# Performance work log

Hardware: AMD Instinct MI355X
Metric: run time of the kernel (lower is better)

Reference implementation:

```python
import jax, jax.numpy as jnp
import numpy as np

GN_EPS = 1e-5
G = 8          # SKA groups
SKS3 = 27      # sks**3


def _aff(x, s, b):
    # folded BatchNorm (eval): per-channel scale + shift on NCDHW tensor
    return x * s[None, :, None, None, None] + b[None, :, None, None, None]


def _c1(x, w):
    # 1x1x1 conv as channel GEMM; w: [O, I]
    return jnp.einsum('bcdhw,oc->bodhw', x, w)


def _dw5(x, w):
    # depthwise 5x5x5 conv, pad=2; w: [C, 1, 5, 5, 5]
    return jax.lax.conv_general_dilated(
        x, w, window_strides=(1, 1, 1), padding=[(2, 2)] * 3,
        dimension_numbers=('NCDHW', 'OIDHW', 'NCDHW'),
        feature_group_count=x.shape[1])


def setup_inputs() -> dict:
    key = jax.random.key(0)
    ks = jax.random.split(key, 24)
    B, C, D, H, W = 2, 64, 32, 32, 32

    def n(k, shape, scale=1.0):
        return jax.random.normal(k, shape, jnp.float32) * scale

    def u(k, shape):
        return jax.random.uniform(k, shape, jnp.float32, 0.5, 1.5)

    return {
        'x': n(ks[0], (B, C, D, H, W)),
        'w1': n(ks[1], (32, 64), 64 ** -0.5),
        's1': u(ks[2], (32,)), 'b1': n(ks[3], (32,), 0.1),
        'w2': n(ks[4], (32, 1, 5, 5, 5), 125 ** -0.5),
        's2': u(ks[5], (32,)), 'b2': n(ks[6], (32,), 0.1),
        'w3': n(ks[7], (32, 32), 32 ** -0.5),
        's3': u(ks[8], (32,)), 'b3': n(ks[9], (32,), 0.1),
        'w4': n(ks[10], (216, 32), 32 ** -0.5), 'b4': n(ks[11], (216,), 0.1),
        'gn_g': u(ks[12], (216,)), 'gn_b': n(ks[13], (216,), 0.1),
        'bn_s': u(ks[14], (64,)), 'bn_b': n(ks[15], (64,), 0.1),
        'pw1_w': n(ks[16], (128, 64), 64 ** -0.5),
        'pw1_s': u(ks[17], (128,)), 'pw1_b': n(ks[18], (128,), 0.1),
        'pw2_w': n(ks[19], (64, 128), 128 ** -0.5),
        'pw2_s': u(ks[20], (64,)), 'pw2_b': n(ks[21], (64,), 0.1),
    }


def reference(x, w1, s1, b1, w2, s2, b2, w3, s3, b3, w4, b4,
              gn_g, gn_b, bn_s, bn_b,
              pw1_w, pw1_s, pw1_b, pw2_w, pw2_s, pw2_b):
    B, C, D, H, W = x.shape

    # ---- LKP3D: dynamic kernel generation ----
    a = jax.nn.relu(_aff(_c1(x, w1), s1, b1))          # cv1 + BN + ReLU
    a = _aff(_dw5(a, w2), s2, b2)                      # cv2 (5^3 dw) + BN
    a = jax.nn.relu(_aff(_c1(a, w3), s3, b3))          # cv3 + BN + ReLU
    wk = _c1(a, w4) + b4[None, :, None, None, None]    # cv4: [B,216,D,H,W]
    # GroupNorm: num_groups = dim//groups = 8, channels = 216
    g = wk.reshape(B, G, SKS3, D, H, W)
    mu = g.mean(axis=(2, 3, 4, 5), keepdims=True)
    var = g.var(axis=(2, 3, 4, 5), keepdims=True)
    g = (g - mu) * jax.lax.rsqrt(var + GN_EPS)
    wk = g.reshape(B, G * SKS3, D, H, W) * gn_g[None, :, None, None, None] \
         + gn_b[None, :, None, None, None]
    wk = wk.reshape(B, G, SKS3, D, H, W)               # [B, G, 27, D, H, W]

    # ---- SKA3D: apply dynamic kernels (27 shifted copies, grouped) ----
    offs = [(di, hi, wi) for di in (-1, 0, 1) for hi in (-1, 0, 1) for wi in (-1, 0, 1)]
    patches = jnp.stack(
        [jnp.roll(x, (-di, -hi, -wi), axis=(2, 3, 4)) for di, hi, wi in offs],
        axis=2)                                        # [B, C, 27, D, H, W]
    p = patches.reshape(B, G, C // G, SKS3, D, H, W)
    sk = jnp.einsum('bgckdhw,bgkdhw->bgcdhw', p, wk).reshape(B, C, D, H, W)

    y = _aff(sk, bn_s, bn_b) + x                       # LSConv BN + residual

    # ---- FFN (residual): pw1 + BN + ReLU + pw2 + BN ----
    f = jax.nn.relu(_aff(_c1(y, pw1_w), pw1_s, pw1_b))
    f = _aff(_c1(f, pw2_w), pw2_s, pw2_b)
    return y + f
```

## Files before the change

kernel.cpp:

```cpp
#include <hip/hip_runtime.h>

#define SPAT 32768
#define BATCH 2
#define GN_EPS 1e-5f

__device__ __forceinline__ void fma4(float4& a, const float4& v, float w) {
    a.x = fmaf(v.x, w, a.x); a.y = fmaf(v.y, w, a.y);
    a.z = fmaf(v.z, w, a.z); a.w = fmaf(v.w, w, a.w);
}

template <int CIN, int NO, bool RELU, bool AFF>
__global__ __launch_bounds__(256) void k_c1(
    const float* __restrict__ in, const float* __restrict__ w,
    const float* __restrict__ sc, const float* __restrict__ bi,
    float* __restrict__ out, int Cout)
{
    int q = blockIdx.x * 256 + threadIdx.x;
    int s = q * 4;
    int o0 = blockIdx.y * NO, b = blockIdx.z;
    const float* ip = in + (size_t)b * CIN * SPAT + s;
    float4 acc[NO];
#pragma unroll
    for (int i = 0; i < NO; ++i) acc[i] = {0.f, 0.f, 0.f, 0.f};
#pragma unroll 4
    for (int c = 0; c < CIN; ++c) {
        float4 v = *(const float4*)(ip + (size_t)c * SPAT);
#pragma unroll
        for (int i = 0; i < NO; ++i)
            fma4(acc[i], v, w[(o0 + i) * CIN + c]);
    }
#pragma unroll
    for (int i = 0; i < NO; ++i) {
        int o = o0 + i;
        float scale = AFF ? sc[o] : 1.f;
        float shift = bi[o];
        float4 r = acc[i];
        r.x = r.x * scale + shift; r.y = r.y * scale + shift;
        r.z = r.z * scale + shift; r.w = r.w * scale + shift;
        if (RELU) {
            r.x = fmaxf(r.x, 0.f); r.y = fmaxf(r.y, 0.f);
            r.z = fmaxf(r.z, 0.f); r.w = fmaxf(r.w, 0.f);
        }
        *(float4*)(out + ((size_t)b * Cout + o) * SPAT + s) = r;
    }
}

__global__ __launch_bounds__(256) void k_gram(
    const float* __restrict__ a, float* __restrict__ partial)
{
    __shared__ float lds[32 * 257];
    int blk = blockIdx.x, b = blockIdx.z;
    const float* ap = a + (size_t)b * 32 * SPAT + blk * 256;
    for (int i = threadIdx.x; i < 32 * 64; i += 256) {
        int m = i >> 6, p4 = (i & 63) * 4;
        float4 v = *(const float4*)(ap + (size_t)m * SPAT + p4);
        lds[m * 257 + p4 + 0] = v.x; lds[m * 257 + p4 + 1] = v.y;
        lds[m * 257 + p4 + 2] = v.z; lds[m * 257 + p4 + 3] = v.w;
    }
    __syncthreads();
    float* outp = partial + (size_t)(b * 128 + blk) * 1056;
#pragma unroll
    for (int it = 0; it < 4; ++it) {
        int pid = threadIdx.x + it * 256;
        const float* pa = &lds[(pid >> 5) * 257];
        const float* pb = &lds[(pid & 31) * 257];
        float acc = 0.f;
#pragma unroll 8
        for (int p = 0; p < 256; ++p) acc = fmaf(pa[p], pb[p], acc);
        outp[pid] = acc;
    }
    if (threadIdx.x < 32) {
        const float* pa = &lds[threadIdx.x * 257];
        float scc = 0.f;
#pragma unroll 8
        for (int p = 0; p < 256; ++p) scc += pa[p];
        outp[1024 + threadIdx.x] = scc;
    }
}

__global__ __launch_bounds__(512) void k_stats(
    const float* __restrict__ partial, const float* __restrict__ w4,
    const float* __restrict__ b4, float* __restrict__ stats)
{
    __shared__ float G[2 * 1056];
    __shared__ float sred[432], ssred[432];
    for (int e = threadIdx.x; e < 2 * 1056; e += 512) {
        int b = e / 1056, pid = e % 1056;
        float acc = 0.f;
#pragma unroll 8
        for (int blk = 0; blk < 128; ++blk)
            acc += partial[(size_t)(b * 128 + blk) * 1056 + pid];
        G[e] = acc;
    }
    __syncthreads();
    if (threadIdx.x < 432) {
        int t = threadIdx.x;
        int b = t / 216, r = t % 216, g = r / 27, k = r % 27;
        const float* wk = w4 + (g * 27 + k) * 32;
        float wreg[32];
#pragma unroll
        for (int m = 0; m < 32; ++m) wreg[m] = wk[m];
        const float* Gb = &G[b * 1056];
        const float* Sb = &G[b * 1056 + 1024];
        float sk = 0.f, ssk = 0.f;
#pragma unroll
        for (int m = 0; m < 32; ++m) {
            sk = fmaf(wreg[m], Sb[m], sk);
            float dot = 0.f;
#pragma unroll
            for (int mm = 0; mm < 32; ++mm)
                dot = fmaf(wreg[mm], Gb[m * 32 + mm], dot);
            ssk = fmaf(wreg[m], dot, ssk);
        }
        float bb = b4[g * 27 + k];
        float NN = (float)SPAT;
        ssk += 2.f * bb * sk + NN * bb * bb;
        sk  += NN * bb;
        sred[t] = sk; ssred[t] = ssk;
    }
    __syncthreads();
    if (threadIdx.x < 16) {
        int bg = threadIdx.x;
        float s = 0.f, ss = 0.f;
        for (int k = 0; k < 27; ++k) { s += sred[bg * 27 + k]; ss += ssred[bg * 27 + k]; }
        float N27 = 27.f * (float)SPAT;
        float mu = s / N27;
        float var = ss / N27 - mu * mu;
        stats[bg * 2 + 0] = mu;
        stats[bg * 2 + 1] = rsqrtf(var + GN_EPS);
    }
}

__global__ __launch_bounds__(256) void k_ska(
    const float* __restrict__ x, const float* __restrict__ wk,
    const float* __restrict__ stats,
    const float* __restrict__ gn_g, const float* __restrict__ gn_b,
    const float* __restrict__ bn_s, const float* __restrict__ bn_b,
    float* __restrict__ y)
{
    int q = blockIdx.x * 256 + threadIdx.x;
    int s = q * 4;
    int g = blockIdx.y, b = blockIdx.z;
    int bg = b * 8 + g;
    float mu  = stats[bg * 2 + 0];
    float inv = stats[bg * 2 + 1];
    int d = s >> 10, h = (s >> 5) & 31, w0 = s & 31;
    int lane = threadIdx.x & 63;
    int xl_src = (lane & 56) | ((lane + 7) & 7);
    int xr_src = (lane & 56) | ((lane + 1) & 7);
    const float* xg = x + ((size_t)(b * 64 + g * 8)) * SPAT;
    const float* wp = wk + ((size_t)(b * 216 + g * 27)) * SPAT + s;

    float4 acc[8];
    float4 xc[8];
#pragma unroll
    for (int c = 0; c < 8; ++c) acc[c] = {0.f, 0.f, 0.f, 0.f};

#pragma unroll
    for (int kd = 0; kd < 3; ++kd) {
        int zd = (d + kd + 31) & 31;
#pragma unroll
        for (int kh = 0; kh < 3; ++kh) {
            int zh = (h + kh + 31) & 31;
            int kbase = (kd * 3 + kh) * 3;
            float wn[3][4];
#pragma unroll
            for (int kw = 0; kw < 3; ++kw) {
                int kk = kbase + kw;
                float4 wq = *(const float4*)(wp + (size_t)kk * SPAT);
                float A = gn_g[g * 27 + kk] * inv;
                float B = gn_b[g * 27 + kk] - mu * A;
                wn[kw][0] = wq.x * A + B;
                wn[kw][1] = wq.y * A + B;
                wn[kw][2] = wq.z * A + B;
                wn[kw][3] = wq.w * A + B;
            }
            int rowoff = zd * 1024 + zh * 32;
            bool center = (kd == 1) && (kh == 1);
#pragma unroll
            for (int c = 0; c < 8; ++c) {
                float4 m = *(const float4*)(xg + (size_t)c * SPAT + rowoff + w0);
                if (center) xc[c] = m;
                float xl = __shfl(m.w, xl_src, 64);
                float xr = __shfl(m.x, xr_src, 64);
                float win[6] = {xl, m.x, m.y, m.z, m.w, xr};
#pragma unroll
                for (int kw = 0; kw < 3; ++kw) {
                    acc[c].x = fmaf(win[0 + kw], wn[kw][0], acc[c].x);
                    acc[c].y = fmaf(win[1 + kw], wn[kw][1], acc[c].y);
                    acc[c].z = fmaf(win[2 + kw], wn[kw][2], acc[c].z);
                    acc[c].w = fmaf(win[3 + kw], wn[kw][3], acc[c].w);
                }
            }
        }
    }
#pragma unroll
    for (int c = 0; c < 8; ++c) {
        int ch = g * 8 + c;
        float bs = bn_s[ch], bb = bn_b[ch];
        float4 r;
        r.x = acc[c].x * bs + bb + xc[c].x;
        r.y = acc[c].y * bs + bb + xc[c].y;
        r.z = acc[c].z * bs + bb + xc[c].z;
        r.w = acc[c].w * bs + bb + xc[c].w;
        *(float4*)(y + ((size_t)(b * 64 + ch)) * SPAT + s) = r;
    }
}

__global__ __launch_bounds__(256) void k_dw5(
    const float* __restrict__ in, const float* __restrict__ w2,
    const float* __restrict__ s2, const float* __restrict__ b2,
    float* __restrict__ out)
{
    __shared__ float lds[8 * 36 * 40];
    int tid = threadIdx.x;
    int d0 = blockIdx.x * 4;
    int c = blockIdx.y, b = blockIdx.z;
    const float* ip = in + ((size_t)(b * 32 + c)) * SPAT;

    float4 z = {0.f, 0.f, 0.f, 0.f};
    for (int i = tid; i < 8 * 36 * 40 / 4; i += 256)
        ((float4*)lds)[i] = z;
    __syncthreads();
    for (int i = tid; i < 8 * 256; i += 256) {
        int p = i >> 8, rem = i & 255;
        int r = rem >> 3, c4 = (rem & 7) * 4;
        int d = d0 - 2 + p;
        if (d >= 0 && d < 32) {
            float4 v = *(const float4*)(ip + d * 1024 + r * 32 + c4);
            *(float4*)&lds[p * 1440 + (r + 2) * 40 + (c4 + 4)] = v;
        }
    }
    __syncthreads();

    float scl = s2[c], shf = b2[c];
    const float* wt = w2 + c * 125;
#pragma unroll
    for (int k = 0; k < 4; ++k) {
        int j = tid + k * 256;
        int pd = j >> 8, rem = j & 255;
        int hr = rem >> 3, w4i = (rem & 7) * 4;
        float4 acc = {0.f, 0.f, 0.f, 0.f};
#pragma unroll
        for (int kd = 0; kd < 5; ++kd) {
            const float* pl = &lds[(pd + kd) * 1440];
#pragma unroll
            for (int kh = 0; kh < 5; ++kh) {
                const float* row = pl + (hr + kh) * 40 + w4i;
                float4 r0 = *(const float4*)(row);
                float4 r1 = *(const float4*)(row + 4);
                float4 r2 = *(const float4*)(row + 8);
                float win[12] = {r0.x, r0.y, r0.z, r0.w,
                                 r1.x, r1.y, r1.z, r1.w,
                                 r2.x, r2.y, r2.z, r2.w};
#pragma unroll
                for (int kw = 0; kw < 5; ++kw) {
                    float wv = wt[kd * 25 + kh * 5 + kw];
                    acc.x = fmaf(wv, win[2 + 0 + kw], acc.x);
                    acc.y = fmaf(wv, win[2 + 1 + kw], acc.y);
                    acc.z = fmaf(wv, win[2 + 2 + kw], acc.z);
                    acc.w = fmaf(wv, win[2 + 3 + kw], acc.w);
                }
            }
        }
        acc.x = acc.x * scl + shf; acc.y = acc.y * scl + shf;
        acc.z = acc.z * scl + shf; acc.w = acc.w * scl + shf;
        *(float4*)(out + ((size_t)(b * 32 + c)) * SPAT
                   + (d0 + pd) * 1024 + hr * 32 + w4i) = acc;
    }
}

template <int NO>
__global__ __launch_bounds__(256) void k_pw2_out(
    const float* __restrict__ f1, const float* __restrict__ w,
    const float* __restrict__ sc, const float* __restrict__ bi,
    const float* __restrict__ yres, float* __restrict__ out)
{
    int q = blockIdx.x * 256 + threadIdx.x;
    int s = q * 4;
    int o0 = blockIdx.y * NO, b = blockIdx.z;
    const float* ip = f1 + (size_t)b * 128 * SPAT + s;
    float4 acc[NO];
#pragma unroll
    for (int i = 0; i < NO; ++i) acc[i] = {0.f, 0.f, 0.f, 0.f};
#pragma unroll 4
    for (int c = 0; c < 128; ++c) {
        float4 v = *(const float4*)(ip + (size_t)c * SPAT);
#pragma unroll
        for (int i = 0; i < NO; ++i)
            fma4(acc[i], v, w[(o0 + i) * 128 + c]);
    }
#pragma unroll
    for (int i = 0; i < NO; ++i) {
        int o = o0 + i;
        float scale = sc[o], shift = bi[o];
        float4 yv = *(const float4*)(yres + ((size_t)(b * 64 + o)) * SPAT + s);
        float4 r = acc[i];
        r.x = r.x * scale + shift + yv.x;
        r.y = r.y * scale + shift + yv.y;
        r.z = r.z * scale + shift + yv.z;
        r.w = r.w * scale + shift + yv.w;
        *(float4*)(out + ((size_t)(b * 64 + o)) * SPAT + s) = r;
    }
}

extern "C" void kernel_launch(void* const* d_in, const int* in_sizes, int n_in,
                              void* d_out, int out_size, void* d_ws, size_t ws_size,
                              hipStream_t stream)
{
    const float* x     = (const float*)d_in[0];
    const float* w1    = (const float*)d_in[1];
    const float* s1    = (const float*)d_in[2];
    const float* b1    = (const float*)d_in[3];
    const float* w2    = (const float*)d_in[4];
    const float* s2    = (const float*)d_in[5];
    const float* b2    = (const float*)d_in[6];
    const float* w3    = (const float*)d_in[7];
    const float* s3    = (const float*)d_in[8];
    const float* b3    = (const float*)d_in[9];
    const float* w4    = (const float*)d_in[10];
    const float* b4    = (const float*)d_in[11];
    const float* gn_g  = (const float*)d_in[12];
    const float* gn_b  = (const float*)d_in[13];
    const float* bn_s  = (const float*)d_in[14];
    const float* bn_b  = (const float*)d_in[15];
    const float* pw1_w = (const float*)d_in[16];
    const float* pw1_s = (const float*)d_in[17];
    const float* pw1_b = (const float*)d_in[18];
    const float* pw2_w = (const float*)d_in[19];
    const float* pw2_s = (const float*)d_in[20];
    const float* pw2_b = (const float*)d_in[21];

    float* ws    = (float*)d_ws;
    float* a1    = ws;
    float* a2    = a1 + (size_t)BATCH * 32 * SPAT;
    float* yb    = ws;
    float* wkb   = ws + (size_t)BATCH * 64 * SPAT;
    float* f1    = wkb;
    float* part  = wkb + (size_t)BATCH * 216 * SPAT;
    float* stats = part + (size_t)256 * 1056;

    dim3 blk(256);
    k_c1<64, 4, true, true><<<dim3(SPAT / 1024, 8, BATCH), blk, 0, stream>>>(
        x, w1, s1, b1, a1, 32);
    k_dw5<<<dim3(8, 32, BATCH), blk, 0, stream>>>(a1, w2, s2, b2, a2);
    k_c1<32, 4, true, true><<<dim3(SPAT / 1024, 8, BATCH), blk, 0, stream>>>(
        a2, w3, s3, b3, a1, 32);
    k_gram<<<dim3(128, 1, BATCH), blk, 0, stream>>>(a1, part);
    k_stats<<<dim3(1), dim3(512), 0, stream>>>(part, w4, b4, stats);
    k_c1<32, 8, false, false><<<dim3(SPAT / 1024, 27, BATCH), blk, 0, stream>>>(
        a1, w4, nullptr, b4, wkb, 216);
    k_ska<<<dim3(SPAT / 1024, 8, BATCH), blk, 0, stream>>>(
        x, wkb, stats, gn_g, gn_b, bn_s, bn_b, yb);
    k_c1<64, 8, true, true><<<dim3(SPAT / 1024, 16, BATCH), blk, 0, stream>>>(
        yb, pw1_w, pw1_s, pw1_b, f1, 128);
    k_pw2_out<8><<<dim3(SPAT / 1024, 8, BATCH), blk, 0, stream>>>(
        f1, pw2_w, pw2_s, pw2_b, yb, (float*)d_out);
}
```

Baseline: 270.2 us.

## Fuse cv4 dynamic-kernel generation into SKA kernel via shared memory

The cv4 1x1 conv that produced the 216-channel dynamic kernel tensor is now computed inside the SKA kernel. Each block computes its group's 27 normalized weights for 512 voxels into LDS, then applies them. This removes writing and re-reading the large wk buffer from global memory. It costs an extra kernel-weight GEMM per block, about 55KB of LDS per block (which lowers occupancy), and 2-wide rather than 4-wide vectors. The pw1 and pw2 launches are also retuned to 4 outputs per block with twice as many blocks.

```diff
diff --git a/kernel.cpp b/kernel.cpp
--- a/kernel.cpp
+++ b/kernel.cpp
@@ -7,6 +7,9 @@
 __device__ __forceinline__ void fma4(float4& a, const float4& v, float w) {
     a.x = fmaf(v.x, w, a.x); a.y = fmaf(v.y, w, a.y);
     a.z = fmaf(v.z, w, a.z); a.w = fmaf(v.w, w, a.w);
+}
+__device__ __forceinline__ void fma2(float2& a, const float2& v, float w) {
+    a.x = fmaf(v.x, w, a.x); a.y = fmaf(v.y, w, a.y);
 }
 
 template <int CIN, int NO, bool RELU, bool AFF>
@@ -131,30 +134,59 @@
     }
 }
 
-__global__ __launch_bounds__(256) void k_ska(
-    const float* __restrict__ x, const float* __restrict__ wk,
+__global__ __launch_bounds__(256) void k_ska_f(
+    const float* __restrict__ x, const float* __restrict__ a1,
+    const float* __restrict__ w4, const float* __restrict__ b4,
     const float* __restrict__ stats,
     const float* __restrict__ gn_g, const float* __restrict__ gn_b,
     const float* __restrict__ bn_s, const float* __restrict__ bn_b,
     float* __restrict__ y)
 {
-    int q = blockIdx.x * 256 + threadIdx.x;
-    int s = q * 4;
-    int g = blockIdx.y, b = blockIdx.z;
+    __shared__ float wn[27 * 514];
+    int chunk = blockIdx.x, g = blockIdx.y, b = blockIdx.z;
+    int base = chunk * 512;
+    int t = threadIdx.x;
     int bg = b * 8 + g;
     float mu  = stats[bg * 2 + 0];
     float inv = stats[bg * 2 + 1];
+    const float* wg = w4 + g * 27 * 32;
+
+    {
+        const float* ap = a1 + (size_t)b * 32 * SPAT + base + 2 * t;
+        float2 acc[27];
+#pragma unroll
+        for (int k = 0; k < 27; ++k) acc[k] = {0.f, 0.f};
+#pragma unroll 4
+        for (int c = 0; c < 32; ++c) {
+            float2 v = *(const float2*)(ap + (size_t)c * SPAT);
+#pragma unroll
+            for (int k = 0; k < 27; ++k)
+                fma2(acc[k], v, wg[k * 32 + c]);
+        }
+#pragma unroll
+        for (int k = 0; k < 27; ++k) {
+            int o = g * 27 + k;
+            float A = gn_g[o] * inv;
+            float B = fmaf(b4[o] - mu, A, gn_b[o]);
+            float2 r;
+            r.x = fmaf(acc[k].x, A, B);
+            r.y = fmaf(acc[k].y, A, B);
+            *(float2*)&wn[k * 514 + 2 * t] = r;
+        }
+    }
+    __syncthreads();
+
+    int s = base + 2 * t;
     int d = s >> 10, h = (s >> 5) & 31, w0 = s & 31;
-    int lane = threadIdx.x & 63;
-    int xl_src = (lane & 56) | ((lane + 7) & 7);
-    int xr_src = (lane & 56) | ((lane + 1) & 7);
-    const float* xg = x + ((size_t)(b * 64 + g * 8)) * SPAT;
-    const float* wp = wk + ((size_t)(b * 216 + g * 27)) * SPAT + s;
-
-    float4 acc[8];
-    float4 xc[8];
-#pragma unroll
-    for (int c = 0; c < 8; ++c) acc[c] = {0.f, 0.f, 0.f, 0.f};
+    int lane = t & 63;
+    int xl_src = (lane & 48) | ((lane + 15) & 15);
+    int xr_src = (lane & 48) | ((lane + 1) & 15);
+    const float* xg = x + (size_t)(b * 64 + g * 8) * SPAT;
+
+    float2 acc2[8];
+    float2 xc2[8];
+#pragma unroll
+    for (int c = 0; c < 8; ++c) acc2[c] = {0.f, 0.f};
 
 #pragma unroll
     for (int kd = 0; kd < 3; ++kd) {
@@ -163,33 +195,23 @@
         for (int kh = 0; kh < 3; ++kh) {
             int zh = (h + kh + 31) & 31;
             int kbase = (kd * 3 + kh) * 3;
-            float wn[3][4];
-#pragma unroll
-            for (int kw = 0; kw < 3; ++kw) {
-                int kk = kbase + kw;
-                float4 wq = *(const float4*)(wp + (size_t)kk * SPAT);
-                float A = gn_g[g * 27 + kk] * inv;
-                float B = gn_b[g * 27 + kk] - mu * A;
-                wn[kw][0] = wq.x * A + B;
-                wn[kw][1] = wq.y * A + B;
-                wn[kw][2] = wq.z * A + B;
-                wn[kw][3] = wq.w * A + B;
-            }
-            int rowoff = zd * 1024 + zh * 32;
+            float2 wt[3];
+#pragma unroll
+            for (int kw = 0; kw < 3; ++kw)
+                wt[kw] = *(const float2*)&wn[(kbase + kw) * 514 + 2 * t];
+            int rowoff = zd * 1024 + zh * 32 + w0;
             bool center = (kd == 1) && (kh == 1);
 #pragma unroll
             for (int c = 0; c < 8; ++c) {
-                float4 m = *(const float4*)(xg + (size_t)c * SPAT + rowoff + w0);
-                if (center) xc[c] = m;
-                float xl = __shfl(m.w, xl_src, 64);
+                float2 m = *(const float2*)(xg + (size_t)c * SPAT + rowoff);
+                if (center) xc2[c] = m;
+                float xl = __shfl(m.y, xl_src, 64);
                 float xr = __shfl(m.x, xr_src, 64);
-                float win[6] = {xl, m.x, m.y, m.z, m.w, xr};
+                float win[4] = {xl, m.x, m.y, xr};
 #pragma unroll
                 for (int kw = 0; kw < 3; ++kw) {
-                    acc[c].x = fmaf(win[0 + kw], wn[kw][0], acc[c].x);
-                    acc[c].y = fmaf(win[1 + kw], wn[kw][1], acc[c].y);
-                    acc[c].z = fmaf(win[2 + kw], wn[kw][2], acc[c].z);
-                    acc[c].w = fmaf(win[3 + kw], wn[kw][3], acc[c].w);
+                    acc2[c].x = fmaf(win[kw],     wt[kw].x, acc2[c].x);
+                    acc2[c].y = fmaf(win[kw + 1], wt[kw].y, acc2[c].y);
                 }
             }
         }
@@ -198,12 +220,10 @@
     for (int c = 0; c < 8; ++c) {
         int ch = g * 8 + c;
         float bs = bn_s[ch], bb = bn_b[ch];
-        float4 r;
-        r.x = acc[c].x * bs + bb + xc[c].x;
-        r.y = acc[c].y * bs + bb + xc[c].y;
-        r.z = acc[c].z * bs + bb + xc[c].z;
-        r.w = acc[c].w * bs + bb + xc[c].w;
-        *(float4*)(y + ((size_t)(b * 64 + ch)) * SPAT + s) = r;
+        float2 r;
+        r.x = acc2[c].x * bs + bb + xc2[c].x;
+        r.y = acc2[c].y * bs + bb + xc2[c].y;
+        *(float2*)(y + ((size_t)(b * 64 + ch)) * SPAT + s) = r;
     }
 }
 
@@ -334,10 +354,9 @@
     float* ws    = (float*)d_ws;
     float* a1    = ws;
     float* a2    = a1 + (size_t)BATCH * 32 * SPAT;
-    float* yb    = ws;
-    float* wkb   = ws + (size_t)BATCH * 64 * SPAT;
-    float* f1    = wkb;
-    float* part  = wkb + (size_t)BATCH * 216 * SPAT;
+    float* yb    = a2 + (size_t)BATCH * 32 * SPAT;
+    float* f1    = yb + (size_t)BATCH * 64 * SPAT;
+    float* part  = f1 + (size_t)BATCH * 128 * SPAT;
     float* stats = part + (size_t)256 * 1056;
 
     dim3 blk(256);
@@ -348,12 +367,10 @@
         a2, w3, s3, b3, a1, 32);
     k_gram<<<dim3(128, 1, BATCH), blk, 0, stream>>>(a1, part);
     k_stats<<<dim3(1), dim3(512), 0, stream>>>(part, w4, b4, stats);
-    k_c1<32, 8, false, false><<<dim3(SPAT / 1024, 27, BATCH), blk, 0, stream>>>(
-        a1, w4, nullptr, b4, wkb, 216);
-    k_ska<<<dim3(SPAT / 1024, 8, BATCH), blk, 0, stream>>>(
-        x, wkb, stats, gn_g, gn_b, bn_s, bn_b, yb);
-    k_c1<64, 8, true, true><<<dim3(SPAT / 1024, 16, BATCH), blk, 0, stream>>>(
+    k_ska_f<<<dim3(SPAT / 512, 8, BATCH), blk, 0, stream>>>(
+        x, a1, w4, b4, stats, gn_g, gn_b, bn_s, bn_b, yb);
+    k_c1<64, 4, true, true><<<dim3(SPAT / 1024, 32, BATCH), blk, 0, stream>>>(
         yb, pw1_w, pw1_s, pw1_b, f1, 128);
-    k_pw2_out<8><<<dim3(SPAT / 1024, 8, BATCH), blk, 0, stream>>>(
+    k_pw2_out<4><<<dim3(SPAT / 1024, 16, BATCH), blk, 0, stream>>>(
         f1, pw2_w, pw2_s, pw2_b, yb, (float*)d_out);
 }
```

After: 270.5 us. About the same (+0.1%).
